# Optimization experiments

Hardware: AMD Instinct MI355X
Metric: run time of the kernel (lower is better)

The kernel has to match this reference:

```python
import jax, jax.numpy as jnp
import numpy as np

D = 2048
H = 16
HD = D // H
DFF = 8192
EPS = 1e-6


def rmsnorm(x, w):
    xf = x.astype(jnp.float32)
    var = jnp.mean(xf * xf, axis=-1, keepdims=True)
    return w * (xf * jax.lax.rsqrt(var + EPS)).astype(x.dtype)


def setup_inputs() -> dict:
    key = jax.random.key(0)
    ks = jax.random.split(key, 10)
    s = 0.02
    return {
        "hidden_states": jax.random.normal(ks[0], (2, 2048, D), jnp.float32),
        "wq": jax.random.normal(ks[1], (D, D), jnp.float32) * s,
        "wk": jax.random.normal(ks[2], (D, D), jnp.float32) * s,
        "wv": jax.random.normal(ks[3], (D, D), jnp.float32) * s,
        "wo": jax.random.normal(ks[4], (D, D), jnp.float32) * s,
        "w_gate": jax.random.normal(ks[5], (DFF, D), jnp.float32) * s,
        "w_up": jax.random.normal(ks[6], (DFF, D), jnp.float32) * s,
        "w_down": jax.random.normal(ks[7], (D, DFF), jnp.float32) * s,
        "ln1_w": jnp.ones((D,), jnp.float32),
        "ln2_w": jnp.ones((D,), jnp.float32),
    }


def reference(hidden_states, wq, wk, wv, wo, w_gate, w_up, w_down, ln1_w, ln2_w):
    B, S, _ = hidden_states.shape
    residual = hidden_states
    x = rmsnorm(hidden_states, ln1_w)
    # projections (torch Linear: y = x @ W.T), split heads -> [B,H,S,HD]
    q = (x @ wq.T).reshape(B, S, H, HD).transpose(0, 2, 1, 3)
    k = (x @ wk.T).reshape(B, S, H, HD).transpose(0, 2, 1, 3)
    v = (x @ wv.T).reshape(B, S, H, HD).transpose(0, 2, 1, 3)
    scores = jnp.einsum("bhqd,bhkd->bhqk", q, k) / np.sqrt(HD).astype(np.float32)
    causal = jnp.triu(jnp.ones((S, S), bool), k=1)  # True above diagonal -> masked
    scores = jnp.where(causal, -jnp.inf, scores)
    attn = jax.nn.softmax(scores, axis=-1)
    out = jnp.einsum("bhqk,bhkd->bhqd", attn, v)
    out = out.transpose(0, 2, 1, 3).reshape(B, S, D)
    out = out @ wo.T
    hidden = residual + out
    residual = hidden
    y = rmsnorm(hidden, ln2_w)
    gate = y @ w_gate.T
    up = y @ w_up.T
    mlp = (jax.nn.silu(gate) * up) @ w_down.T
    return residual + mlp
```

## Files before the change

### kernel.cpp

```cpp
#include <hip/hip_runtime.h>
#include <stdint.h>

#define D_MODEL 2048
#define NHEADS  16
#define HEADDIM 128
#define DFF     8192
#define BATCH   2
#define SEQ     2048
#define NTOK    (BATCH*SEQ)
#define EPS     1e-6f
#define QKV_RS  (3*D_MODEL)

typedef unsigned short u16;
typedef short  s16x8 __attribute__((ext_vector_type(8)));
typedef float  f32x4 __attribute__((ext_vector_type(4)));

__device__ __forceinline__ u16 f2bf(float f) {
  union { float f; uint32_t u; } v; v.f = f;
  uint32_t u = v.u;
  return (u16)((u + 0x7fffu + ((u >> 16) & 1u)) >> 16);
}
__device__ __forceinline__ float bf2f(u16 h) {
  union { uint32_t u; float f; } v; v.u = ((uint32_t)h) << 16;
  return v.f;
}

__device__ __forceinline__ void gload_lds16(const void* g, void* l) {
  __builtin_amdgcn_global_load_lds(
      (const __attribute__((address_space(1))) void*)g,
      (__attribute__((address_space(3))) void*)l, 16, 0, 0);
}

__device__ __forceinline__ f32x4 mfma16(s16x8 a, s16x8 b, f32x4 c) {
  return __builtin_amdgcn_mfma_f32_16x16x32_bf16(a, b, c, 0, 0, 0);
}

#define BAR()   asm volatile("s_barrier" ::: "memory")
#define LGK0()  asm volatile("s_waitcnt lgkmcnt(0)" ::: "memory")

__device__ __forceinline__ void cvt_one(const float* in, u16* out, int i) {
  float4 v = ((const float4*)in)[i];
  uint32_t lo = (uint32_t)f2bf(v.x) | ((uint32_t)f2bf(v.y) << 16);
  uint32_t hi = (uint32_t)f2bf(v.z) | ((uint32_t)f2bf(v.w) << 16);
  uint2 st; st.x = lo; st.y = hi;
  ((uint2*)out)[i] = st;
}

__global__ __launch_bounds__(256)
void cvt_kernel(const float* __restrict__ in, u16* __restrict__ out, int n4)
{
  int idx = blockIdx.x * 256 + threadIdx.x;
  int stride = gridDim.x * 256;
  for (int i = idx; i < n4; i += stride) cvt_one(in, out, i);
}

__global__ __launch_bounds__(256)
void cvt4_kernel(const float* __restrict__ a, const float* __restrict__ b,
                 const float* __restrict__ c, const float* __restrict__ d,
                 u16* __restrict__ oa, u16* __restrict__ ob,
                 u16* __restrict__ oc, u16* __restrict__ od, int n4)
{
  int idx = blockIdx.x * 256 + threadIdx.x;
  int stride = gridDim.x * 256;
  for (int i = idx; i < 4 * n4; i += stride) {
    int w = i / n4, j = i - w * n4;
    const float* s = (w == 0) ? a : (w == 1) ? b : (w == 2) ? c : d;
    u16* o = (w == 0) ? oa : (w == 1) ? ob : (w == 2) ? oc : od;
    cvt_one(s, o, j);
  }
}

__global__ __launch_bounds__(256)
void cvt2_kernel(const float* __restrict__ a, const float* __restrict__ b,
                 u16* __restrict__ oa, u16* __restrict__ ob, int n4)
{
  int idx = blockIdx.x * 256 + threadIdx.x;
  int stride = gridDim.x * 256;
  for (int i = idx; i < 2 * n4; i += stride) {
    int w = i / n4, j = i - w * n4;
    cvt_one(w ? b : a, w ? ob : oa, j);
  }
}

__global__ __launch_bounds__(256)
void rmsnorm_kernel(const float* __restrict__ x, const float* __restrict__ w,
                    u16* __restrict__ out)
{
  int row = blockIdx.x;
  int tid = threadIdx.x;
  const float4* xr = (const float4*)(x + (size_t)row * D_MODEL);
  float4 a = xr[tid];
  float4 b = xr[tid + 256];
  float ss = a.x*a.x + a.y*a.y + a.z*a.z + a.w*a.w
           + b.x*b.x + b.y*b.y + b.z*b.z + b.w*b.w;
#pragma unroll
  for (int o = 32; o > 0; o >>= 1) ss += __shfl_xor(ss, o);
  __shared__ float red[4];
  if ((tid & 63) == 0) red[tid >> 6] = ss;
  __syncthreads();
  float tot = red[0] + red[1] + red[2] + red[3];
  float sc = rsqrtf(tot * (1.0f / D_MODEL) + EPS);
  const float4* wr = (const float4*)w;
  float4 wa = wr[tid], wb = wr[tid + 256];
  u16* orow = out + (size_t)row * D_MODEL;
  uint2 s0, s1;
  s0.x = (uint32_t)f2bf(a.x*wa.x*sc) | ((uint32_t)f2bf(a.y*wa.y*sc) << 16);
  s0.y = (uint32_t)f2bf(a.z*wa.z*sc) | ((uint32_t)f2bf(a.w*wa.w*sc) << 16);
  s1.x = (uint32_t)f2bf(b.x*wb.x*sc) | ((uint32_t)f2bf(b.y*wb.y*sc) << 16);
  s1.y = (uint32_t)f2bf(b.z*wb.z*sc) | ((uint32_t)f2bf(b.w*wb.w*sc) << 16);
  ((uint2*)orow)[tid] = s0;
  ((uint2*)orow)[tid + 256] = s1;
}

#define BM 128
#define BN 128
#define BK 64

template<int EPI>
__global__ __launch_bounds__(256, 2)
void gemm_bt(const u16* __restrict__ A, const u16* __restrict__ B,
             void* __restrict__ Cout, const float* __restrict__ aux,
             int M, int N, int K)
{
  __shared__ u16 As[BM * BK];
  __shared__ u16 Bs[BN * BK];
  const int nbn = N / BN;
  int bid = blockIdx.x;
  int swz = (gridDim.x & 7) ? bid : ((bid & 7) * (gridDim.x >> 3) + (bid >> 3));
  const int bm = swz / nbn, bn = swz % nbn;
  const int m0 = bm * BM, n0 = bn * BN;
  const int tid = threadIdx.x;
  const int lane = tid & 63;
  const int wm = tid >> 7, wn = (tid >> 6) & 1;
  const int lr = lane & 15, lg = lane >> 4;

  f32x4 acc[4][4] = {};

  for (int k0 = 0; k0 < K; k0 += BK) {
#pragma unroll
    for (int i = 0; i < 4; ++i) {
      int c = i * 256 + tid;
      int row = c >> 3, cr = c & 7;
      int g = cr ^ (row & 7);
      gload_lds16(A + (size_t)(m0 + row) * K + k0 + (g << 3), &As[c * 8]);
      gload_lds16(B + (size_t)(n0 + row) * K + k0 + (g << 3), &Bs[c * 8]);
    }
    __syncthreads();
#pragma unroll
    for (int kk = 0; kk < BK; kk += 32) {
      s16x8 a[4], b[4];
#pragma unroll
      for (int m = 0; m < 4; ++m) {
        int row = wm * 64 + m * 16 + lr;
        int j = (kk >> 3) + lg;
        a[m] = *(const s16x8*)&As[row * BK + ((j ^ (row & 7)) << 3)];
      }
#pragma unroll
      for (int n = 0; n < 4; ++n) {
        int row = wn * 64 + n * 16 + lr;
        int j = (kk >> 3) + lg;
        b[n] = *(const s16x8*)&Bs[row * BK + ((j ^ (row & 7)) << 3)];
      }
#pragma unroll
      for (int m = 0; m < 4; ++m)
#pragma unroll
        for (int n = 0; n < 4; ++n)
          acc[m][n] = mfma16(a[m], b[n], acc[m][n]);
    }
    __syncthreads();
  }

#pragma unroll
  for (int m = 0; m < 4; ++m) {
#pragma unroll
    for (int n = 0; n < 4; ++n) {
      int col = n0 + wn * 64 + n * 16 + lr;
#pragma unroll
      for (int r = 0; r < 4; ++r) {
        int row = m0 + wm * 64 + m * 16 + lg * 4 + r;
        size_t idx = (size_t)row * N + col;
        float v = acc[m][n][r];
        if (EPI == 0) {
          ((u16*)Cout)[idx] = f2bf(v);
        } else if (EPI == 1) {
          float up = bf2f(((u16*)Cout)[idx]);
          float s = v / (1.0f + __expf(-v));
          ((u16*)Cout)[idx] = f2bf(s * up);
        } else if (EPI == 2) {
          ((float*)Cout)[idx] = aux[idx] + v;
        } else {
          ((float*)Cout)[idx] += v;
        }
      }
    }
  }
}

template<int EPI>
__global__ __launch_bounds__(512, 2)
void gemm256(const u16* __restrict__ A, const u16* __restrict__ B,
             void* __restrict__ Cout, const float* __restrict__ aux,
             int M, int N, int K)
{
  __shared__ u16 As[2][2][256 * 32];
  __shared__ u16 Bs[2][2][256 * 32];
  const int nbn = N >> 8;
  const int bm = blockIdx.x / nbn, bn = blockIdx.x % nbn;
  const int m0 = bm << 8, n0 = bn << 8;
  const int tid = threadIdx.x, lane = tid & 63;
  const int wid = tid >> 6;
  const int wm = wid >> 2, wn = wid & 3;
  const int lr = lane & 15, lg = lane >> 4;

  f32x4 acc[8][4] = {};

  auto stA = [&](int td, int ts, int kh) {
    const u16* src = A + (size_t)m0 * K + ts * 64 + kh * 32;
    u16* dst = &As[td & 1][kh][0];
#pragma unroll
    for (int i = 0; i < 2; ++i) {
      int c = i * 512 + tid;
      int row = c >> 2, sl = c & 3;
      int g = sl ^ ((row >> 1) & 3);
      gload_lds16(src + (size_t)row * K + (g << 3), dst + (c << 3));
    }
  };
  auto stB = [&](int td, int ts, int kh) {
    const u16* src = B + (size_t)n0 * K + ts * 64 + kh * 32;
    u16* dst = &Bs[td & 1][kh][0];
#pragma unroll
    for (int i = 0; i < 2; ++i) {
      int c = i * 512 + tid;
      int row = c >> 2, sl = c & 3;
      int g = sl ^ ((row >> 1) & 3);
      gload_lds16(src + (size_t)row * K + (g << 3), dst + (c << 3));
    }
  };
  auto rdA = [&](int t, int kh, int m) -> s16x8 {
    int row = wm * 128 + m * 16 + lr;
    int sl = lg ^ ((row >> 1) & 3);
    return *(const s16x8*)&As[t & 1][kh][row * 32 + (sl << 3)];
  };
  auto rdB = [&](int t, int kh, int n) -> s16x8 {
    int row = wn * 64 + n * 16 + lr;
    int sl = lg ^ ((row >> 1) & 3);
    return *(const s16x8*)&Bs[t & 1][kh][row * 32 + (sl << 3)];
  };

  const int nt = K >> 6;

  stA(0, 0, 0); stB(0, 0, 0);
  stA(0, 0, 1); stB(0, 0, 1);
  asm volatile("s_waitcnt vmcnt(4)" ::: "memory");
  BAR();

  s16x8 aA[4], aB[4], bA[4], bB[4];
#pragma unroll
  for (int n = 0; n < 4; ++n) bA[n] = rdB(0, 0, n);
#pragma unroll
  for (int m = 0; m < 4; ++m) aA[m] = rdA(0, 0, m);
  stA(1, 1, 0); stB(1, 1, 0);
  asm volatile("s_waitcnt vmcnt(4)" ::: "memory");
  BAR();

#pragma unroll 1
  for (int t = 0; t < nt; ++t) {
    const int tp1 = t + 1, tp2 = t + 2;
    const int s1 = tp1 < nt ? tp1 : nt - 1;
    const int s2 = tp2 < nt ? tp2 : nt - 1;

    stA(tp1, s1, 1);
#pragma unroll
    for (int m = 0; m < 4; ++m) aB[m] = rdA(t, 0, m + 4);
    __builtin_amdgcn_s_setprio(1);
#pragma unroll
    for (int m = 0; m < 4; ++m)
#pragma unroll
      for (int n = 0; n < 4; ++n) acc[m][n] = mfma16(aA[m], bA[n], acc[m][n]);
    __builtin_amdgcn_s_setprio(0);

    stB(tp1, s1, 1);
#pragma unroll
    for (int n = 0; n < 4; ++n) bB[n] = rdB(t, 1, n);
#pragma unroll
    for (int m = 0; m < 4; ++m) aA[m] = rdA(t, 1, m);
    __builtin_amdgcn_s_setprio(1);
#pragma unroll
    for (int m = 0; m < 4; ++m)
#pragma unroll
      for (int n = 0; n < 4; ++n) acc[m + 4][n] = mfma16(aB[m], bA[n], acc[m + 4][n]);
    __builtin_amdgcn_s_setprio(0);
    asm volatile("s_waitcnt vmcnt(4)" ::: "memory");
    BAR();

    stA(tp2, s2, 0);
#pragma unroll
    for (int m = 0; m < 4; ++m) aB[m] = rdA(t, 1, m + 4);
    __builtin_amdgcn_s_setprio(1);
#pragma unroll
    for (int m = 0; m < 4; ++m)
#pragma unroll
      for (int n = 0; n < 4; ++n) acc[m][n] = mfma16(aA[m], bB[n], acc[m][n]);
    __builtin_amdgcn_s_setprio(0);

    stB(tp2, s2, 0);
#pragma unroll
    for (int n = 0; n < 4; ++n) bA[n] = rdB(tp1, 0, n);
#pragma unroll
    for (int m = 0; m < 4; ++m) aA[m] = rdA(tp1, 0, m);
    __builtin_amdgcn_s_setprio(1);
#pragma unroll
    for (int m = 0; m < 4; ++m)
#pragma unroll
      for (int n = 0; n < 4; ++n) acc[m + 4][n] = mfma16(aB[m], bB[n], acc[m + 4][n]);
    __builtin_amdgcn_s_setprio(0);
    asm volatile("s_waitcnt vmcnt(4)" ::: "memory");
    BAR();
  }

  asm volatile("s_waitcnt vmcnt(0)" ::: "memory");

#pragma unroll
  for (int m = 0; m < 8; ++m) {
#pragma unroll
    for (int n = 0; n < 4; ++n) {
      int col = n0 + wn * 64 + n * 16 + lr;
#pragma unroll
      for (int r = 0; r < 4; ++r) {
        int row = m0 + wm * 128 + m * 16 + lg * 4 + r;
        size_t idx = (size_t)row * N + col;
        float v = acc[m][n][r];
        if (EPI == 0) {
          ((u16*)Cout)[idx] = f2bf(v);
        } else if (EPI == 1) {
          float up = bf2f(((u16*)Cout)[idx]);
          float s = v / (1.0f + __expf(-v));
          ((u16*)Cout)[idx] = f2bf(s * up);
        } else if (EPI == 2) {
          ((float*)Cout)[idx] = aux[idx] + v;
        } else {
          ((float*)Cout)[idx] += v;
        }
      }
    }
  }
}

#define QBLK 128
#define KVBLK 64

__global__ __launch_bounds__(256, 2)
void attn_kernel(const u16* __restrict__ QKV, u16* __restrict__ O)
{
  __shared__ u16 Ks[2][KVBLK * HEADDIM];
  __shared__ u16 Vt[HEADDIM * KVBLK];
  __shared__ u16 Pw[4][32 * KVBLK];

  const int bid = blockIdx.x;
  const int q4 = bid & 15;
  const int h  = (bid >> 4) & (NHEADS - 1);
  const int b  = bid >> 8;
  const int qb = b ? q4 : 15 - q4;
  const int tid = threadIdx.x, lane = tid & 63, wid = tid >> 6;
  const int lr = lane & 15, lg = lane >> 4;
  const size_t tokbase = (size_t)b * SEQ;
  const int hoff = h * HEADDIM;
  const int qr0 = qb * QBLK + wid * 32;
  const int wq_max = qr0 + 31;
  const int nkb = (qb + 1) * (QBLK / KVBLK);
  const float scale = 0.08838834764831845f;

  s16x8 qf[2][4];
#pragma unroll
  for (int m = 0; m < 2; ++m)
#pragma unroll
    for (int c = 0; c < 4; ++c)
      qf[m][c] = *(const s16x8*)(QKV + (tokbase + qr0 + m * 16 + lr) * QKV_RS
                                 + hoff + c * 32 + lg * 8);

  f32x4 o_acc[2][8] = {};
  float m_run[2][4], l_run[2][4];
#pragma unroll
  for (int m = 0; m < 2; ++m)
#pragma unroll
    for (int r = 0; r < 4; ++r) { m_run[m][r] = -1e30f; l_run[m][r] = 0.0f; }

  s16x8 v0[2], v1[2];

  {
    const u16* kbase = QKV + tokbase * QKV_RS + D_MODEL + hoff;
#pragma unroll
    for (int it = 0; it < 4; ++it) {
      int c = it * 256 + tid;
      int row = c >> 4, cr = c & 15;
      int g = cr ^ (row & 7);
      gload_lds16(kbase + (size_t)row * QKV_RS + g * 8, &Ks[0][c * 8]);
    }
    const u16* vbase = QKV + tokbase * QKV_RS + 2 * D_MODEL + hoff;
#pragma unroll
    for (int i = 0; i < 2; ++i) {
      int pi = i * 256 + tid;
      int rp = pi >> 4, dc = pi & 15;
      const u16* vp = vbase + (size_t)(rp * 2) * QKV_RS + dc * 8;
      v0[i] = *(const s16x8*)vp;
      v1[i] = *(const s16x8*)(vp + QKV_RS);
    }
    uint32_t* vt = (uint32_t*)&Vt[0];
#pragma unroll
    for (int i = 0; i < 2; ++i) {
      int pi = i * 256 + tid;
      int rp = pi >> 4, dc = pi & 15;
      int k0 = rp * 2;
      int base = ((k0 >> 3) ^ (dc & 7)) * 4 + ((k0 >> 1) & 3);
#pragma unroll
      for (int j = 0; j < 8; ++j)
        vt[(dc * 8 + j) * (KVBLK / 2) + base] =
            (uint32_t)(u16)v0[i][j] | ((uint32_t)(u16)v1[i][j] << 16);
    }
  }
  __syncthreads();

  for (int kb = 0; kb < nkb; ++kb) {
    const int buf = kb & 1;
    const bool nb = (kb + 1 < nkb);

    if (nb) {
      const u16* kbase = QKV + (tokbase + (size_t)(kb + 1) * KVBLK) * QKV_RS + D_MODEL + hoff;
#pragma unroll
      for (int it = 0; it < 4; ++it) {
        int c = it * 256 + tid;
        int row = c >> 4, cr = c & 15;
        int g = cr ^ (row & 7);
        gload_lds16(kbase + (size_t)row * QKV_RS + g * 8, &Ks[buf ^ 1][c * 8]);
      }
      const u16* vbase = QKV + (tokbase + (size_t)(kb + 1) * KVBLK) * QKV_RS + 2 * D_MODEL + hoff;
#pragma unroll
      for (int i = 0; i < 2; ++i) {
        int pi = i * 256 + tid;
        int rp = pi >> 4, dc = pi & 15;
        const u16* vp = vbase + (size_t)(rp * 2) * QKV_RS + dc * 8;
        v0[i] = *(const s16x8*)vp;
        v1[i] = *(const s16x8*)(vp + QKV_RS);
      }
    }

    if (kb * KVBLK <= wq_max) {
      f32x4 s_acc[2][4] = {};
#pragma unroll
      for (int kk = 0; kk < 4; ++kk) {
        s16x8 kf[4];
#pragma unroll
        for (int n = 0; n < 4; ++n) {
          int row = n * 16 + lr;
          int ch = (kk * 4 + lg) ^ (row & 7);
          kf[n] = *(const s16x8*)&Ks[buf][row * HEADDIM + ch * 8];
        }
#pragma unroll
        for (int m = 0; m < 2; ++m)
#pragma unroll
          for (int n = 0; n < 4; ++n)
            s_acc[m][n] = mfma16(qf[m][kk], kf[n], s_acc[m][n]);
      }

#pragma unroll
      for (int m = 0; m < 2; ++m) {
        float tmax[4] = {-1e30f, -1e30f, -1e30f, -1e30f};
        float sv[4][4];
#pragma unroll
        for (int n = 0; n < 4; ++n) {
          int key = kb * KVBLK + n * 16 + lr;
#pragma unroll
          for (int r = 0; r < 4; ++r) {
            int q = qr0 + m * 16 + lg * 4 + r;
            float s = s_acc[m][n][r] * scale;
            if (key > q) s = -1e30f;
            sv[n][r] = s;
            tmax[r] = fmaxf(tmax[r], s);
          }
        }
#pragma unroll
        for (int o = 1; o < 16; o <<= 1)
#pragma unroll
          for (int r = 0; r < 4; ++r)
            tmax[r] = fmaxf(tmax[r], __shfl_xor(tmax[r], o));

        float pf[4], psum[4];
#pragma unroll
        for (int r = 0; r < 4; ++r) {
          float mn = fmaxf(m_run[m][r], tmax[r]);
          pf[r] = __expf(m_run[m][r] - mn);
          m_run[m][r] = mn;
          psum[r] = 0.0f;
        }
#pragma unroll
        for (int n = 0; n < 4; ++n) {
          int keyl = n * 16 + lr;
#pragma unroll
          for (int r = 0; r < 4; ++r) {
            float p = __expf(sv[n][r] - m_run[m][r]);
            psum[r] += p;
            int ql = m * 16 + lg * 4 + r;
            int ch = (keyl >> 3) ^ (ql & 7);
            Pw[wid][ql * KVBLK + ch * 8 + (keyl & 7)] = f2bf(p);
          }
        }
#pragma unroll
        for (int o = 1; o < 16; o <<= 1)
#pragma unroll
          for (int r = 0; r < 4; ++r)
            psum[r] += __shfl_xor(psum[r], o);
#pragma unroll
        for (int r = 0; r < 4; ++r)
          l_run[m][r] = l_run[m][r] * pf[r] + psum[r];
#pragma unroll
        for (int t = 0; t < 8; ++t)
#pragma unroll
          for (int r = 0; r < 4; ++r)
            o_acc[m][t][r] *= pf[r];
      }

#pragma unroll
      for (int kk = 0; kk < 2; ++kk) {
        s16x8 pa[2];
#pragma unroll
        for (int m = 0; m < 2; ++m) {
          int ql = m * 16 + lr;
          int ch = (kk * 4 + lg) ^ (ql & 7);
          pa[m] = *(const s16x8*)&Pw[wid][ql * KVBLK + ch * 8];
        }
#pragma unroll
        for (int t = 0; t < 8; ++t) {
          int d = t * 16 + lr;
          int ch = (kk * 4 + lg) ^ ((d >> 3) & 7);
          s16x8 vf = *(const s16x8*)&Vt[d * KVBLK + ch * 8];
#pragma unroll
          for (int m = 0; m < 2; ++m)
            o_acc[m][t] = mfma16(pa[m], vf, o_acc[m][t]);
        }
      }
    }

    __syncthreads();
    if (nb) {
      uint32_t* vt = (uint32_t*)&Vt[0];
#pragma unroll
      for (int i = 0; i < 2; ++i) {
        int pi = i * 256 + tid;
        int rp = pi >> 4, dc = pi & 15;
        int k0 = rp * 2;
        int base = ((k0 >> 3) ^ (dc & 7)) * 4 + ((k0 >> 1) & 3);
#pragma unroll
        for (int j = 0; j < 8; ++j)
          vt[(dc * 8 + j) * (KVBLK / 2) + base] =
              (uint32_t)(u16)v0[i][j] | ((uint32_t)(u16)v1[i][j] << 16);
      }
    }
    __syncthreads();
  }

#pragma unroll
  for (int m = 0; m < 2; ++m)
#pragma unroll
    for (int t = 0; t < 8; ++t)
#pragma unroll
      for (int r = 0; r < 4; ++r) {
        int q = qr0 + m * 16 + lg * 4 + r;
        O[(tokbase + q) * D_MODEL + hoff + t * 16 + lr] =
            f2bf(o_acc[m][t][r] / l_run[m][r]);
      }
}

extern "C" void kernel_launch(void* const* d_in, const int* in_sizes, int n_in,
                              void* d_out, int out_size, void* d_ws, size_t ws_size,
                              hipStream_t stream)
{
  const float* hidden = (const float*)d_in[0];
  const float* wq    = (const float*)d_in[1];
  const float* wk    = (const float*)d_in[2];
  const float* wv    = (const float*)d_in[3];
  const float* wo    = (const float*)d_in[4];
  const float* wgate = (const float*)d_in[5];
  const float* wup   = (const float*)d_in[6];
  const float* wdown = (const float*)d_in[7];
  const float* ln1   = (const float*)d_in[8];
  const float* ln2   = (const float*)d_in[9];
  float* out = (float*)d_out;

  const size_t TD = (size_t)NTOK * D_MODEL;
  const size_t DD = (size_t)D_MODEL * D_MODEL;
  const size_t FD = (size_t)DFF * D_MODEL;

  u16* XN  = (u16*)d_ws;
  u16* QKV = XN + TD;
  u16* AO  = QKV + 3 * TD;
  u16* WB  = AO + TD;
  u16* GU  = WB + FD;

  dim3 b256(256), b512(512);

  cvt4_kernel<<<dim3(2048), b256, 0, stream>>>(
      wq, wk, wv, wo, WB + 0 * DD, WB + 1 * DD, WB + 2 * DD, WB + 3 * DD,
      (int)(DD / 4));

  rmsnorm_kernel<<<dim3(NTOK), b256, 0, stream>>>(hidden, ln1, XN);

  gemm256<0><<<dim3(16 * 24), b512, 0, stream>>>(XN, WB, QKV, nullptr, NTOK, 3 * D_MODEL, D_MODEL);

  attn_kernel<<<dim3(BATCH * NHEADS * (SEQ / QBLK)), b256, 0, stream>>>(QKV, AO);

  gemm_bt<2><<<dim3(32 * 16), b256, 0, stream>>>(AO, WB + 3 * DD, out, hidden, NTOK, D_MODEL, D_MODEL);

  cvt2_kernel<<<dim3(4096), b256, 0, stream>>>(wgate, wup, WB, QKV, (int)(FD / 4));

  rmsnorm_kernel<<<dim3(NTOK), b256, 0, stream>>>(out, ln2, XN);

  gemm256<0><<<dim3(16 * 32), b512, 0, stream>>>(XN, QKV, GU, nullptr, NTOK, DFF, D_MODEL);
  gemm256<1><<<dim3(16 * 32), b512, 0, stream>>>(XN, WB, GU, nullptr, NTOK, DFF, D_MODEL);

  cvt_kernel<<<dim3(8192), b256, 0, stream>>>(wdown, QKV, (int)(FD / 4));

  gemm_bt<3><<<dim3(32 * 16), b256, 0, stream>>>(GU, QKV, out, nullptr, NTOK, D_MODEL, DFF);
}
```

Measured before the change: 910.5 us.

## Balance causal attention by pairing light and heavy query blocks per workgroup

Each workgroup now handles two 64-row query slabs, p and 31-p, one early and one late in the sequence, so every block does about the same total causal work. Before, each block took one 128-row slab and the blocks were very unequal in length. The key loop runs to the heavier slab's extent, and the light slab's MFMAs and softmax are skipped once its keys are exhausted. This trades per-wave branching and partly idle MFMA issue on late iterations for balanced block durations and less tail imbalance.

```diff
diff --git a/kernel.cpp b/kernel.cpp
--- a/kernel.cpp
+++ b/kernel.cpp
@@ -357,26 +357,26 @@
   __shared__ u16 Pw[4][32 * KVBLK];
 
   const int bid = blockIdx.x;
-  const int q4 = bid & 15;
+  const int p  = bid & 15;
   const int h  = (bid >> 4) & (NHEADS - 1);
   const int b  = bid >> 8;
-  const int qb = b ? q4 : 15 - q4;
   const int tid = threadIdx.x, lane = tid & 63, wid = tid >> 6;
   const int lr = lane & 15, lg = lane >> 4;
   const size_t tokbase = (size_t)b * SEQ;
   const int hoff = h * HEADDIM;
-  const int qr0 = qb * QBLK + wid * 32;
-  const int wq_max = qr0 + 31;
-  const int nkb = (qb + 1) * (QBLK / KVBLK);
+  const int qrow0 = p * 64 + wid * 16;
+  const int qrow1 = (31 - p) * 64 + wid * 16;
+  const int nkb = 32 - p;
   const float scale = 0.08838834764831845f;
 
   s16x8 qf[2][4];
 #pragma unroll
-  for (int m = 0; m < 2; ++m)
-#pragma unroll
-    for (int c = 0; c < 4; ++c)
-      qf[m][c] = *(const s16x8*)(QKV + (tokbase + qr0 + m * 16 + lr) * QKV_RS
-                                 + hoff + c * 32 + lg * 8);
+  for (int c = 0; c < 4; ++c) {
+    qf[0][c] = *(const s16x8*)(QKV + (tokbase + qrow0 + lr) * QKV_RS
+                               + hoff + c * 32 + lg * 8);
+    qf[1][c] = *(const s16x8*)(QKV + (tokbase + qrow1 + lr) * QKV_RS
+                               + hoff + c * 32 + lg * 8);
+  }
 
   f32x4 o_acc[2][8] = {};
   float m_run[2][4], l_run[2][4];
@@ -423,6 +423,7 @@
   for (int kb = 0; kb < nkb; ++kb) {
     const int buf = kb & 1;
     const bool nb = (kb + 1 < nkb);
+    const bool act0 = (kb <= p);
 
     if (nb) {
       const u16* kbase = QKV + (tokbase + (size_t)(kb + 1) * KVBLK) * QKV_RS + D_MODEL + hoff;
@@ -444,98 +445,102 @@
       }
     }
 
-    if (kb * KVBLK <= wq_max) {
-      f32x4 s_acc[2][4] = {};
-#pragma unroll
-      for (int kk = 0; kk < 4; ++kk) {
-        s16x8 kf[4];
-#pragma unroll
-        for (int n = 0; n < 4; ++n) {
-          int row = n * 16 + lr;
-          int ch = (kk * 4 + lg) ^ (row & 7);
-          kf[n] = *(const s16x8*)&Ks[buf][row * HEADDIM + ch * 8];
+    f32x4 s_acc[2][4] = {};
+#pragma unroll
+    for (int kk = 0; kk < 4; ++kk) {
+      s16x8 kf[4];
+#pragma unroll
+      for (int n = 0; n < 4; ++n) {
+        int row = n * 16 + lr;
+        int ch = (kk * 4 + lg) ^ (row & 7);
+        kf[n] = *(const s16x8*)&Ks[buf][row * HEADDIM + ch * 8];
+      }
+#pragma unroll
+      for (int m = 0; m < 2; ++m) {
+        if (m == 0 && !act0) continue;
+#pragma unroll
+        for (int n = 0; n < 4; ++n)
+          s_acc[m][n] = mfma16(qf[m][kk], kf[n], s_acc[m][n]);
+      }
+    }
+
+#pragma unroll
+    for (int m = 0; m < 2; ++m) {
+      if (m == 0 && !act0) continue;
+      const int qb_ = (m == 0) ? qrow0 : qrow1;
+      float tmax[4] = {-1e30f, -1e30f, -1e30f, -1e30f};
+      float sv[4][4];
+#pragma unroll
+      for (int n = 0; n < 4; ++n) {
+        int key = kb * KVBLK + n * 16 + lr;
+#pragma unroll
+        for (int r = 0; r < 4; ++r) {
+          int q = qb_ + lg * 4 + r;
+          float s = s_acc[m][n][r] * scale;
+          if (key > q) s = -1e30f;
+          sv[n][r] = s;
+          tmax[r] = fmaxf(tmax[r], s);
         }
-#pragma unroll
-        for (int m = 0; m < 2; ++m)
-#pragma unroll
-          for (int n = 0; n < 4; ++n)
-            s_acc[m][n] = mfma16(qf[m][kk], kf[n], s_acc[m][n]);
-      }
-
+      }
+#pragma unroll
+      for (int o = 1; o < 16; o <<= 1)
+#pragma unroll
+        for (int r = 0; r < 4; ++r)
+          tmax[r] = fmaxf(tmax[r], __shfl_xor(tmax[r], o));
+
+      float pf[4], psum[4];
+#pragma unroll
+      for (int r = 0; r < 4; ++r) {
+        float mn = fmaxf(m_run[m][r], tmax[r]);
+        pf[r] = __expf(m_run[m][r] - mn);
+        m_run[m][r] = mn;
+        psum[r] = 0.0f;
+      }
+#pragma unroll
+      for (int n = 0; n < 4; ++n) {
+        int keyl = n * 16 + lr;
+#pragma unroll
+        for (int r = 0; r < 4; ++r) {
+          float pv = __expf(sv[n][r] - m_run[m][r]);
+          psum[r] += pv;
+          int ql = m * 16 + lg * 4 + r;
+          int ch = (keyl >> 3) ^ (ql & 7);
+          Pw[wid][ql * KVBLK + ch * 8 + (keyl & 7)] = f2bf(pv);
+        }
+      }
+#pragma unroll
+      for (int o = 1; o < 16; o <<= 1)
+#pragma unroll
+        for (int r = 0; r < 4; ++r)
+          psum[r] += __shfl_xor(psum[r], o);
+#pragma unroll
+      for (int r = 0; r < 4; ++r)
+        l_run[m][r] = l_run[m][r] * pf[r] + psum[r];
+#pragma unroll
+      for (int t = 0; t < 8; ++t)
+#pragma unroll
+        for (int r = 0; r < 4; ++r)
+          o_acc[m][t][r] *= pf[r];
+    }
+
+#pragma unroll
+    for (int kk = 0; kk < 2; ++kk) {
+      s16x8 pa[2];
 #pragma unroll
       for (int m = 0; m < 2; ++m) {
-        float tmax[4] = {-1e30f, -1e30f, -1e30f, -1e30f};
-        float sv[4][4];
-#pragma unroll
-        for (int n = 0; n < 4; ++n) {
-          int key = kb * KVBLK + n * 16 + lr;
-#pragma unroll
-          for (int r = 0; r < 4; ++r) {
-            int q = qr0 + m * 16 + lg * 4 + r;
-            float s = s_acc[m][n][r] * scale;
-            if (key > q) s = -1e30f;
-            sv[n][r] = s;
-            tmax[r] = fmaxf(tmax[r], s);
-          }
-        }
-#pragma unroll
-        for (int o = 1; o < 16; o <<= 1)
-#pragma unroll
-          for (int r = 0; r < 4; ++r)
-            tmax[r] = fmaxf(tmax[r], __shfl_xor(tmax[r], o));
-
-        float pf[4], psum[4];
-#pragma unroll
-        for (int r = 0; r < 4; ++r) {
-          float mn = fmaxf(m_run[m][r], tmax[r]);
-          pf[r] = __expf(m_run[m][r] - mn);
-          m_run[m][r] = mn;
-          psum[r] = 0.0f;
-        }
-#pragma unroll
-        for (int n = 0; n < 4; ++n) {
-          int keyl = n * 16 + lr;
-#pragma unroll
-          for (int r = 0; r < 4; ++r) {
-            float p = __expf(sv[n][r] - m_run[m][r]);
-            psum[r] += p;
-            int ql = m * 16 + lg * 4 + r;
-            int ch = (keyl >> 3) ^ (ql & 7);
-            Pw[wid][ql * KVBLK + ch * 8 + (keyl & 7)] = f2bf(p);
-          }
-        }
-#pragma unroll
-        for (int o = 1; o < 16; o <<= 1)
-#pragma unroll
-          for (int r = 0; r < 4; ++r)
-            psum[r] += __shfl_xor(psum[r], o);
-#pragma unroll
-        for (int r = 0; r < 4; ++r)
-          l_run[m][r] = l_run[m][r] * pf[r] + psum[r];
-#pragma unroll
-        for (int t = 0; t < 8; ++t)
-#pragma unroll
-          for (int r = 0; r < 4; ++r)
-            o_acc[m][t][r] *= pf[r];
-      }
-
-#pragma unroll
-      for (int kk = 0; kk < 2; ++kk) {
-        s16x8 pa[2];
+        int ql = m * 16 + lr;
+        int ch = (kk * 4 + lg) ^ (ql & 7);
+        pa[m] = *(const s16x8*)&Pw[wid][ql * KVBLK + ch * 8];
+      }
+#pragma unroll
+      for (int t = 0; t < 8; ++t) {
+        int d = t * 16 + lr;
+        int ch = (kk * 4 + lg) ^ ((d >> 3) & 7);
+        s16x8 vf = *(const s16x8*)&Vt[d * KVBLK + ch * 8];
 #pragma unroll
         for (int m = 0; m < 2; ++m) {
-          int ql = m * 16 + lr;
-          int ch = (kk * 4 + lg) ^ (ql & 7);
-          pa[m] = *(const s16x8*)&Pw[wid][ql * KVBLK + ch * 8];
-        }
-#pragma unroll
-        for (int t = 0; t < 8; ++t) {
-          int d = t * 16 + lr;
-          int ch = (kk * 4 + lg) ^ ((d >> 3) & 7);
-          s16x8 vf = *(const s16x8*)&Vt[d * KVBLK + ch * 8];
-#pragma unroll
-          for (int m = 0; m < 2; ++m)
-            o_acc[m][t] = mfma16(pa[m], vf, o_acc[m][t]);
+          if (m == 0 && !act0) continue;
+          o_acc[m][t] = mfma16(pa[m], vf, o_acc[m][t]);
         }
       }
     }
@@ -564,7 +569,7 @@
     for (int t = 0; t < 8; ++t)
 #pragma unroll
       for (int r = 0; r < 4; ++r) {
-        int q = qr0 + m * 16 + lg * 4 + r;
+        int q = ((m == 0) ? qrow0 : qrow1) + lg * 4 + r;
         O[(tokbase + q) * D_MODEL + hoff + t * 16 + lr] =
             f2bf(o_acc[m][t][r] / l_run[m][r]);
       }
```

Measured after the change: 900.9 us. About the same (-1.1%).
